# Optimization experiments

Hardware: AMD Instinct MI355X
Metric: run time of the kernel (lower is better)

Reference implementation:

```python
import jax, jax.numpy as jnp
import numpy as np

B, IN, H1, H2, OUT, P = 8192, 1024, 2048, 2048, 1024, 8


def setup_inputs() -> dict:
    key = jax.random.key(0)
    ks = jax.random.split(key, 12)
    s = 0.02
    return {
        "x": jax.random.normal(ks[0], (B, IN), dtype=jnp.float32),
        # layer 1: P expert linears (stacked) + selector
        "W1": jax.random.normal(ks[1], (P, IN, H1), dtype=jnp.float32) * s,
        "b1": jax.random.normal(ks[2], (P, H1), dtype=jnp.float32) * s,
        "S1": jax.random.normal(ks[3], (IN, P), dtype=jnp.float32) * s,
        "sb1": jax.random.normal(ks[4], (P,), dtype=jnp.float32) * s,
        # layer 2
        "W2": jax.random.normal(ks[5], (P, H1, H2), dtype=jnp.float32) * s,
        "b2": jax.random.normal(ks[6], (P, H2), dtype=jnp.float32) * s,
        "S2": jax.random.normal(ks[7], (H1, P), dtype=jnp.float32) * s,
        "sb2": jax.random.normal(ks[8], (P,), dtype=jnp.float32) * s,
        # classifier
        "Wc": jax.random.normal(ks[9], (H2, OUT), dtype=jnp.float32) * s,
        "bc": jax.random.normal(ks[10], (OUT,), dtype=jnp.float32) * s,
    }


def _drn_layer(x, W, b, S, sb):
    # selector + softmax routing probs: [B, P]
    probs = jax.nn.softmax(x @ S + sb, axis=-1)
    # all-expert dense outputs: [B, P, O]
    outs = jnp.einsum('bi,pio->bpo', x, W) + b[None, :, :]
    # soft-weighted combine over experts
    return jnp.einsum('bpo,bp->bo', outs, probs)


def reference(x, W1, b1, S1, sb1, W2, b2, S2, sb2, Wc, bc):
    h = jax.nn.relu(_drn_layer(x, W1, b1, S1, sb1))
    h = jax.nn.relu(_drn_layer(h, W2, b2, S2, sb2))
    return h @ Wc + bc
```

## Files before the change

kernel.cpp:

```cpp
#include <hip/hip_runtime.h>
#include <hip/hip_bf16.h>

#define B_SZ   8192
#define IN_SZ  1024
#define H1_SZ  2048
#define H2_SZ  2048
#define OUT_SZ 1024
#define NP     8

typedef __bf16 bf16x8 __attribute__((ext_vector_type(8)));
typedef float  f32x4  __attribute__((ext_vector_type(4)));

__device__ __forceinline__ void async_ld16(const void* g, void* l) {
    __builtin_amdgcn_global_load_lds(
        (const __attribute__((address_space(1))) unsigned int*)g,
        (__attribute__((address_space(3))) unsigned int*)l,
        16, 0, 0);
}

__device__ __forceinline__ void transpose_body(float (*tile)[33],
                                               const float* __restrict__ in,
                                               __hip_bfloat16* __restrict__ out,
                                               int K, int N, int bx, int by) {
    int n0 = bx * 32, k0 = by * 32;
    int tx = threadIdx.x, ty = threadIdx.y;
#pragma unroll
    for (int j = 0; j < 4; ++j)
        tile[ty + j * 8][tx] = in[(size_t)(k0 + ty + j * 8) * N + (n0 + tx)];
    __syncthreads();
    const int kk = (tx & 15) * 2;
#pragma unroll
    for (int j = 0; j < 2; ++j) {
        int nn = ty + j * 8 + (tx >> 4) * 16;
        __hip_bfloat16 t2[2] = {__float2bfloat16(tile[kk][nn]),
                                __float2bfloat16(tile[kk + 1][nn])};
        unsigned int u;
        __builtin_memcpy(&u, t2, 4);
        *(unsigned int*)(out + (size_t)(n0 + nn) * K + (k0 + kk)) = u;
    }
}

__global__ void prep_k(const float* __restrict__ W1, const float* __restrict__ W2,
                       const float* __restrict__ Wc, const float* __restrict__ x,
                       __hip_bfloat16* __restrict__ W1t, __hip_bfloat16* __restrict__ W2t,
                       __hip_bfloat16* __restrict__ Wct, __hip_bfloat16* __restrict__ xbf) {
    __shared__ float tile[32][33];
    int id = blockIdx.x;
    const int nA = (H1_SZ / 32) * ((NP * IN_SZ) / 32);
    const int nB = (H2_SZ / 32) * ((NP * H1_SZ) / 32);
    const int nC = (OUT_SZ / 32) * (H2_SZ / 32);
    if (id < nA) {
        transpose_body(tile, W1, W1t, NP * IN_SZ, H1_SZ, id % (H1_SZ / 32), id / (H1_SZ / 32));
        return;
    }
    id -= nA;
    if (id < nB) {
        transpose_body(tile, W2, W2t, NP * H1_SZ, H2_SZ, id % (H2_SZ / 32), id / (H2_SZ / 32));
        return;
    }
    id -= nB;
    if (id < nC) {
        transpose_body(tile, Wc, Wct, H2_SZ, OUT_SZ, id % (OUT_SZ / 32), id / (OUT_SZ / 32));
        return;
    }
    id -= nC;
    {
        int t = threadIdx.y * 32 + threadIdx.x;
        size_t i = ((size_t)id * 256 + t) * 8;
        float4 f0 = *(const float4*)(x + i);
        float4 f1 = *(const float4*)(x + i + 4);
        __hip_bfloat16 tt[8] = {
            __float2bfloat16(f0.x), __float2bfloat16(f0.y),
            __float2bfloat16(f0.z), __float2bfloat16(f0.w),
            __float2bfloat16(f1.x), __float2bfloat16(f1.y),
            __float2bfloat16(f1.z), __float2bfloat16(f1.w)};
        uint4 u4;
        __builtin_memcpy(&u4, tt, 16);
        *(uint4*)(xbf + i) = u4;
    }
}

template <typename T>
__global__ void selector_k(const T* __restrict__ in, const float* __restrict__ S,
                           const float* __restrict__ sb, float* __restrict__ probs,
                           float* __restrict__ ratT, int K) {
    int row  = blockIdx.x * blockDim.y + threadIdx.y;
    int lane = threadIdx.x;
    float acc[NP];
#pragma unroll
    for (int p = 0; p < NP; ++p) acc[p] = 0.f;
    const T* xr = in + (size_t)row * K;
    for (int k = lane; k < K; k += 64) {
        float xv;
        if constexpr (sizeof(T) == 2) xv = __bfloat162float(xr[k]);
        else                          xv = (float)xr[k];
        const float* sr = S + (size_t)k * NP;
#pragma unroll
        for (int p = 0; p < NP; ++p) acc[p] += xv * sr[p];
    }
#pragma unroll
    for (int p = 0; p < NP; ++p)
#pragma unroll
        for (int off = 32; off > 0; off >>= 1)
            acc[p] += __shfl_down(acc[p], off, 64);
    if (lane == 0) {
        float v[NP], m = -1e30f;
#pragma unroll
        for (int p = 0; p < NP; ++p) { v[p] = acc[p] + sb[p]; m = fmaxf(m, v[p]); }
        float s = 0.f;
#pragma unroll
        for (int p = 0; p < NP; ++p) { v[p] = expf(v[p] - m); s += v[p]; }
        float inv = 1.f / s;
#pragma unroll
        for (int p = 0; p < NP; ++p) probs[(size_t)row * NP + p] = v[p] * inv;
#pragma unroll
        for (int p = 0; p < NP - 1; ++p) ratT[(size_t)p * B_SZ + row] = v[p] / v[p + 1];
        ratT[(size_t)(NP - 1) * B_SZ + row] = v[NP - 1] * inv;
    }
}

template <int TPS>
__global__ __launch_bounds__(512, 2)
void drn_gemm8_k(const __hip_bfloat16* __restrict__ A, const __hip_bfloat16* __restrict__ Wt,
                 int N, int K, int Kin, const float* __restrict__ ratT,
                 const float* __restrict__ probs, const float* __restrict__ bexp,
                 __hip_bfloat16* __restrict__ C) {
    __shared__ alignas(16) char smem[131072];

    const int tid  = threadIdx.x;
    const int wid  = tid >> 6, lane = tid & 63;
    const int quad = lane >> 4, l16 = lane & 15;
    const int wr = wid >> 2, wc = wid & 3;

    const int g   = blockIdx.x;
    const int cpx = gridDim.x >> 3;
    const int wg  = (g & 7) * cpx + (g >> 3);
    const int nbn = N >> 8;
    const int mb  = wg / nbn, nb = wg % nbn;
    const int m0  = mb * 256, n0 = nb * 256;

    const int arow = tid >> 3;
    const int gsw  = ((tid & 7) ^ (arow & 7)) << 3;
    const __hip_bfloat16* Ag = A  + (size_t)(m0 + arow) * Kin + gsw;
    const __hip_bfloat16* Bg = Wt + (size_t)(n0 + arow) * K + gsw;
    const size_t r64a = (size_t)64 * Kin;
    const size_t r64b = (size_t)64 * K;
    char* aDst = smem + wid * 1024;
    char* bDst = smem + 65536 + wid * 1024;

#define STG_A(dbuf, ksrc, h) do {                                              \
    const __hip_bfloat16* s_ = Ag + (((ksrc) & (TPS - 1)) * 64) + (size_t)(2*(h)) * r64a; \
    char* d_ = aDst + (dbuf) * 32768 + (h) * 16384;                            \
    async_ld16(s_,        d_);                                                 \
    async_ld16(s_ + r64a, d_ + 8192); } while (0)
#define STG_B(dbuf, ksrc, h) do {                                              \
    const __hip_bfloat16* s_ = Bg + ((size_t)(ksrc) * 64) + (size_t)(2*(h)) * r64b; \
    char* d_ = bDst + (dbuf) * 32768 + (h) * 16384;                            \
    async_ld16(s_,        d_);                                                 \
    async_ld16(s_ + r64b, d_ + 8192); } while (0)

    const int csw  = (quad ^ (l16 & 7)) << 4;
    const int aoff = (wr * 128 + l16) * 128 + csw;
    const int boff = 65536 + (wc * 64 + l16) * 128 + csw;

#define LDA(dst, dbuf, m, k) dst = *(const bf16x8*)(smem + (dbuf) * 32768 + ((aoff ^ ((k) << 6)) + (m) * 2048))
#define LDB(dst, dbuf, n, k) dst = *(const bf16x8*)(smem + (dbuf) * 32768 + ((boff ^ ((k) << 6)) + (n) * 2048))

#define LD_AF(dst, dbuf, mq)                               \
    LDA(dst[0][0], dbuf, 2*(mq),     0); LDA(dst[0][1], dbuf, 2*(mq),     1); \
    LDA(dst[1][0], dbuf, 2*(mq) + 1, 0); LDA(dst[1][1], dbuf, 2*(mq) + 1, 1)
#define LD_BF(dst, dbuf, kk)                               \
    LDB(dst[0][kk], dbuf, 0, kk); LDB(dst[1][kk], dbuf, 1, kk); \
    LDB(dst[2][kk], dbuf, 2, kk); LDB(dst[3][kk], dbuf, 3, kk)

#define BAR()                                              \
    __builtin_amdgcn_s_barrier();                          \
    __builtin_amdgcn_sched_barrier(0)

#define VMW(n) asm volatile("s_waitcnt vmcnt(" #n ")" ::: "memory")

#define MF16(afX, bfrX, q) do {                            \
    __builtin_amdgcn_s_setprio(1);                         \
    _Pragma("unroll")                                      \
    for (int ml = 0; ml < 2; ++ml)                         \
      _Pragma("unroll")                                    \
      for (int n_ = 0; n_ < 4; ++n_)                       \
        _Pragma("unroll")                                  \
        for (int k_ = 0; k_ < 2; ++k_)                     \
          acc[2*(q)+ml][n_] = __builtin_amdgcn_mfma_f32_16x16x32_bf16( \
              afX[ml][k_], bfrX[n_][k_], acc[2*(q)+ml][n_], 0, 0, 0);  \
    __builtin_amdgcn_s_setprio(0); } while (0)

    f32x4 zero = {0.f, 0.f, 0.f, 0.f};
    f32x4 acc[8][4];
#pragma unroll
    for (int m = 0; m < 8; ++m)
#pragma unroll
        for (int n = 0; n < 4; ++n) acc[m][n] = zero;

    const int NT = K >> 6;
    const int NI = NT >> 1;

    STG_A(0, 0, 0); STG_A(0, 0, 1);
    STG_B(0, 0, 0); STG_B(0, 0, 1);
    STG_B(1, 1, 0); STG_B(1, 1, 1);
    VMW(4);
    BAR();
    bf16x8 afA[2][2], afB[2][2], bfrA[4][2], bfrB[4][2];
    LD_BF(bfrA, 0, 0); LD_BF(bfrA, 0, 1);
    LD_AF(afA, 0, 0);

    for (int i = 0; i < NI; ++i) {
        const int T  = 2 * i;
        const int k2 = (T + 2 < NT) ? T + 2 : NT - 1;
        const int k3 = (T + 3 < NT) ? T + 3 : NT - 1;

        STG_A(1, T + 1, 0);
        LD_AF(afB, 0, 1);
        BAR(); MF16(afA, bfrA, 0); BAR();
        STG_A(1, T + 1, 1);
        VMW(4);
        LD_AF(afA, 0, 2);
        BAR(); MF16(afB, bfrA, 1); BAR();
        STG_B(0, k2, 0);
        VMW(2);
        LD_AF(afB, 0, 3);
        LD_BF(bfrB, 1, 0);
        BAR(); MF16(afA, bfrA, 2); BAR();
        STG_B(0, k2, 1);
        LD_AF(afA, 1, 0);
        LD_BF(bfrB, 1, 1);
        BAR(); MF16(afB, bfrA, 3); BAR();
        STG_A(0, k2, 0);
        LD_AF(afB, 1, 1);
        BAR(); MF16(afA, bfrB, 0); BAR();
        STG_A(0, k2, 1);
        VMW(4);
        LD_AF(afA, 1, 2);
        BAR(); MF16(afB, bfrB, 1); BAR();
        STG_B(1, k3, 0);
        VMW(2);
        LD_AF(afB, 1, 3);
        LD_BF(bfrA, 0, 0);
        BAR(); MF16(afA, bfrB, 2); BAR();
        STG_B(1, k3, 1);
        LD_AF(afA, 0, 0);
        LD_BF(bfrA, 0, 1);
        BAR(); MF16(afB, bfrB, 3); BAR();

        if (((i + 1) & (TPS / 2 - 1)) == 0) {
            const int p = (i + 1) / (TPS / 2) - 1;
            const float* rp = ratT + (size_t)p * B_SZ + (m0 + wr * 128 + quad * 4);
            f32x4 rr[8];
#pragma unroll
            for (int m = 0; m < 8; ++m) rr[m] = *(const f32x4*)(rp + m * 16);
#pragma unroll
            for (int m = 0; m < 8; ++m)
#pragma unroll
                for (int n = 0; n < 4; ++n)
                    acc[m][n] *= rr[m];
        }
    }

    asm volatile("s_waitcnt vmcnt(0)" ::: "memory");

    const int colb = n0 + wc * 64 + l16;
    float bx[4][NP];
#pragma unroll
    for (int n = 0; n < 4; ++n)
#pragma unroll
        for (int p = 0; p < NP; ++p)
            bx[n][p] = bexp[(size_t)p * N + colb + n * 16];
#pragma unroll
    for (int m = 0; m < 8; ++m) {
#pragma unroll
        for (int r = 0; r < 4; ++r) {
            const int row = m0 + wr * 128 + m * 16 + quad * 4 + r;
            const float* pr = probs + (size_t)row * NP;
            f32x4 p0 = *(const f32x4*)pr;
            f32x4 p1 = *(const f32x4*)(pr + 4);
            float pv[NP] = {p0[0], p0[1], p0[2], p0[3], p1[0], p1[1], p1[2], p1[3]};
#pragma unroll
            for (int n = 0; n < 4; ++n) {
                float bsum = 0.f;
#pragma unroll
                for (int p = 0; p < NP; ++p) bsum += pv[p] * bx[n][p];
                float v = fmaxf(acc[m][n][r] + bsum, 0.f);
                C[(size_t)row * N + colb + n * 16] = __float2bfloat16(v);
            }
        }
    }
#undef STG_A
#undef STG_B
#undef LDA
#undef LDB
#undef LD_AF
#undef LD_BF
#undef BAR
#undef VMW
#undef MF16
}

__global__ __launch_bounds__(256)
void gemm_bt_k(const __hip_bfloat16* __restrict__ A, const __hip_bfloat16* __restrict__ Bt,
               int M, int N, int K, const float* __restrict__ bias, float* __restrict__ C) {
    __shared__ alignas(16) __hip_bfloat16 As[2 * 128 * 32];
    __shared__ alignas(16) __hip_bfloat16 Bs[2 * 128 * 32];
    const int tid  = threadIdx.x;
    const int wid  = tid >> 6, lane = tid & 63;
    const int quad = lane >> 4, l16 = lane & 15;
    const int waveM = (wid >> 1) << 6, waveN = (wid & 1) << 6;
    const int m0 = blockIdx.x * 128, n0 = blockIdx.y * 128;

    f32x4 zero = {0.f, 0.f, 0.f, 0.f};
    f32x4 acc[4][4];
#pragma unroll
    for (int a = 0; a < 4; ++a)
#pragma unroll
        for (int b = 0; b < 4; ++b) acc[a][b] = zero;

    const int srow = tid >> 2;
    const int skc  = (((tid & 3) ^ (srow & 3) ^ ((srow >> 2) & 3)) << 3);
    const __hip_bfloat16* Ag = A  + (size_t)(m0 + srow) * K + skc;
    const __hip_bfloat16* Bg = Bt + (size_t)(n0 + srow) * K + skc;
    const size_t rowStep = (size_t)64 * K;
    __hip_bfloat16* AsB = As + wid * 512;
    __hip_bfloat16* BsB = Bs + wid * 512;
    const int csel = (quad ^ (l16 & 3) ^ ((l16 >> 2) & 3)) << 3;

    async_ld16(Ag,           AsB);
    async_ld16(Ag + rowStep, AsB + 2048);
    async_ld16(Bg,           BsB);
    async_ld16(Bg + rowStep, BsB + 2048);

    for (int kt = 0; kt < K; kt += 32) {
        const int cur = (kt >> 5) & 1;
        __syncthreads();
        if (kt + 32 < K) {
            const int nb = (1 - cur) * 4096;
            async_ld16(Ag + kt + 32,           AsB + nb);
            async_ld16(Ag + kt + 32 + rowStep, AsB + nb + 2048);
            async_ld16(Bg + kt + 32,           BsB + nb);
            async_ld16(Bg + kt + 32 + rowStep, BsB + nb + 2048);
        }
        const __hip_bfloat16* AsC = As + cur * 4096;
        const __hip_bfloat16* BsC = Bs + cur * 4096;
        bf16x8 af[4], bfr[4];
#pragma unroll
        for (int q = 0; q < 4; ++q) {
            af[q]  = *(const bf16x8*)(AsC + (waveM + q * 16 + l16) * 32 + csel);
            bfr[q] = *(const bf16x8*)(BsC + (waveN + q * 16 + l16) * 32 + csel);
        }
#pragma unroll
        for (int tm = 0; tm < 4; ++tm)
#pragma unroll
            for (int tn = 0; tn < 4; ++tn)
                acc[tm][tn] = __builtin_amdgcn_mfma_f32_16x16x32_bf16(
                    af[tm], bfr[tn], acc[tm][tn], 0, 0, 0);
    }

    const int colb = n0 + waveN + l16;
#pragma unroll
    for (int tm = 0; tm < 4; ++tm)
#pragma unroll
        for (int r = 0; r < 4; ++r) {
            int row = m0 + waveM + tm * 16 + quad * 4 + r;
#pragma unroll
            for (int tn = 0; tn < 4; ++tn)
                C[(size_t)row * N + colb + tn * 16] =
                    acc[tm][tn][r] + bias[colb + tn * 16];
        }
}

extern "C" void kernel_launch(void* const* d_in, const int* in_sizes, int n_in,
                              void* d_out, int out_size, void* d_ws, size_t ws_size,
                              hipStream_t stream) {
    const float* x   = (const float*)d_in[0];
    const float* W1  = (const float*)d_in[1];
    const float* b1  = (const float*)d_in[2];
    const float* S1  = (const float*)d_in[3];
    const float* sb1 = (const float*)d_in[4];
    const float* W2  = (const float*)d_in[5];
    const float* b2  = (const float*)d_in[6];
    const float* S2  = (const float*)d_in[7];
    const float* sb2 = (const float*)d_in[8];
    const float* Wc  = (const float*)d_in[9];
    const float* bc  = (const float*)d_in[10];
    float* out = (float*)d_out;

    char* ws = (char*)d_ws;
    size_t off = 0;
    auto alloc = [&](size_t bytes) {
        char* p = ws + off;
        off += (bytes + 255) & ~(size_t)255;
        return p;
    };
    __hip_bfloat16* W1t = (__hip_bfloat16*)alloc((size_t)H1_SZ * (NP * IN_SZ) * 2);
    __hip_bfloat16* W2t = (__hip_bfloat16*)alloc((size_t)H2_SZ * (NP * H1_SZ) * 2);
    __hip_bfloat16* Wct = (__hip_bfloat16*)alloc((size_t)OUT_SZ * H2_SZ * 2);
    float* probs1       = (float*)alloc((size_t)B_SZ * NP * 4);
    float* probs2       = (float*)alloc((size_t)B_SZ * NP * 4);
    float* rat1         = (float*)alloc((size_t)NP * B_SZ * 4);
    float* rat2         = (float*)alloc((size_t)NP * B_SZ * 4);
    __hip_bfloat16* xbf = (__hip_bfloat16*)alloc((size_t)B_SZ * IN_SZ * 2);
    __hip_bfloat16* h1  = (__hip_bfloat16*)alloc((size_t)B_SZ * H1_SZ * 2);
    __hip_bfloat16* h2  = (__hip_bfloat16*)alloc((size_t)B_SZ * H2_SZ * 2);

    const int nPrep = (H1_SZ / 32) * ((NP * IN_SZ) / 32)
                    + (H2_SZ / 32) * ((NP * H1_SZ) / 32)
                    + (OUT_SZ / 32) * (H2_SZ / 32)
                    + (B_SZ * IN_SZ) / (256 * 8);
    prep_k<<<nPrep, dim3(32, 8), 0, stream>>>(W1, W2, Wc, x, W1t, W2t, Wct, xbf);

    selector_k<float><<<B_SZ / 4, dim3(64, 4), 0, stream>>>(x, S1, sb1, probs1, rat1, IN_SZ);
    drn_gemm8_k<16><<<(B_SZ / 256) * (H1_SZ / 256), 512, 0, stream>>>(
        xbf, W1t, H1_SZ, NP * IN_SZ, IN_SZ, rat1, probs1, b1, h1);

    selector_k<__hip_bfloat16><<<B_SZ / 4, dim3(64, 4), 0, stream>>>(h1, S2, sb2, probs2, rat2, H1_SZ);
    drn_gemm8_k<32><<<(B_SZ / 256) * (H2_SZ / 256), 512, 0, stream>>>(
        h1, W2t, H2_SZ, NP * H1_SZ, H1_SZ, rat2, probs2, b2, h2);

    gemm_bt_k<<<dim3(B_SZ / 128, OUT_SZ / 128), 256, 0, stream>>>(
        h2, Wct, B_SZ, OUT_SZ, H2_SZ, bc, out);
}
```

Before: 990.8 us.

## Restructure MFMA main loop into k-half phases with precomputed LDS fragment pointers

Replaces the ping-pong A/B fragment register double-buffering in the fused expert GEMM with a simpler schedule. Each tile now runs four phases, each loading 4 A fragments (plus B fragments for one k-half) and then issuing 16 MFMAs after an explicit lgkmcnt(0) wait. LDS base pointers are precomputed per buffer and k-half to cut address arithmetic, and the global-load wait points move. The aim is to lower register pressure and instruction overhead, at the cost of losing the overlap between LDS reads and MFMA issue within a wave.

```diff
diff --git a/kernel.cpp b/kernel.cpp
--- a/kernel.cpp
+++ b/kernel.cpp
@@ -159,36 +159,43 @@
     async_ld16(s_,        d_);                                                 \
     async_ld16(s_ + r64b, d_ + 8192); } while (0)
 
-    const int csw  = (quad ^ (l16 & 7)) << 4;
-    const int aoff = (wr * 128 + l16) * 128 + csw;
-    const int boff = 65536 + (wc * 64 + l16) * 128 + csw;
-
-#define LDA(dst, dbuf, m, k) dst = *(const bf16x8*)(smem + (dbuf) * 32768 + ((aoff ^ ((k) << 6)) + (m) * 2048))
-#define LDB(dst, dbuf, n, k) dst = *(const bf16x8*)(smem + (dbuf) * 32768 + ((boff ^ ((k) << 6)) + (n) * 2048))
-
-#define LD_AF(dst, dbuf, mq)                               \
-    LDA(dst[0][0], dbuf, 2*(mq),     0); LDA(dst[0][1], dbuf, 2*(mq),     1); \
-    LDA(dst[1][0], dbuf, 2*(mq) + 1, 0); LDA(dst[1][1], dbuf, 2*(mq) + 1, 1)
-#define LD_BF(dst, dbuf, kk)                               \
-    LDB(dst[0][kk], dbuf, 0, kk); LDB(dst[1][kk], dbuf, 1, kk); \
-    LDB(dst[2][kk], dbuf, 2, kk); LDB(dst[3][kk], dbuf, 3, kk)
+    const int csw   = (quad ^ (l16 & 7)) << 4;
+    const int abase = (wr * 128 + l16) * 128 + csw;
+    const int bbase = 65536 + (wc * 64 + l16) * 128 + csw;
+    const char* aB[2][2] = {{smem + abase,         smem + (abase ^ 64)},
+                            {smem + 32768 + abase, smem + 32768 + (abase ^ 64)}};
+    const char* bB[2][2] = {{smem + bbase,         smem + (bbase ^ 64)},
+                            {smem + 32768 + bbase, smem + 32768 + (bbase ^ 64)}};
+
+#define LD_A4(d, mh, kh)                                                        \
+    af[0] = *(const bf16x8*)(aB[d][kh] + ((mh) * 4 + 0) * 2048);                \
+    af[1] = *(const bf16x8*)(aB[d][kh] + ((mh) * 4 + 1) * 2048);                \
+    af[2] = *(const bf16x8*)(aB[d][kh] + ((mh) * 4 + 2) * 2048);                \
+    af[3] = *(const bf16x8*)(aB[d][kh] + ((mh) * 4 + 3) * 2048)
+#define LD_B4(d, kh)                                                            \
+    bfr[0][kh] = *(const bf16x8*)(bB[d][kh] + 0 * 2048);                        \
+    bfr[1][kh] = *(const bf16x8*)(bB[d][kh] + 1 * 2048);                        \
+    bfr[2][kh] = *(const bf16x8*)(bB[d][kh] + 2 * 2048);                        \
+    bfr[3][kh] = *(const bf16x8*)(bB[d][kh] + 3 * 2048)
 
 #define BAR()                                              \
     __builtin_amdgcn_s_barrier();                          \
     __builtin_amdgcn_sched_barrier(0)
 
+#define LGKM0()                                            \
+    asm volatile("s_waitcnt lgkmcnt(0)" ::: "memory");     \
+    __builtin_amdgcn_sched_barrier(0)
+
 #define VMW(n) asm volatile("s_waitcnt vmcnt(" #n ")" ::: "memory")
 
-#define MF16(afX, bfrX, q) do {                            \
+#define MF(mh, kh) do {                                    \
     __builtin_amdgcn_s_setprio(1);                         \
     _Pragma("unroll")                                      \
-    for (int ml = 0; ml < 2; ++ml)                         \
+    for (int ml = 0; ml < 4; ++ml)                         \
       _Pragma("unroll")                                    \
       for (int n_ = 0; n_ < 4; ++n_)                       \
-        _Pragma("unroll")                                  \
-        for (int k_ = 0; k_ < 2; ++k_)                     \
-          acc[2*(q)+ml][n_] = __builtin_amdgcn_mfma_f32_16x16x32_bf16( \
-              afX[ml][k_], bfrX[n_][k_], acc[2*(q)+ml][n_], 0, 0, 0);  \
+        acc[(mh) * 4 + ml][n_] = __builtin_amdgcn_mfma_f32_16x16x32_bf16( \
+            af[ml], bfr[n_][kh], acc[(mh) * 4 + ml][n_], 0, 0, 0);        \
     __builtin_amdgcn_s_setprio(0); } while (0)
 
     f32x4 zero = {0.f, 0.f, 0.f, 0.f};
@@ -206,47 +213,33 @@
     STG_B(1, 1, 0); STG_B(1, 1, 1);
     VMW(4);
     BAR();
-    bf16x8 afA[2][2], afB[2][2], bfrA[4][2], bfrB[4][2];
-    LD_BF(bfrA, 0, 0); LD_BF(bfrA, 0, 1);
-    LD_AF(afA, 0, 0);
+
+    bf16x8 af[4], bfr[4][2];
 
     for (int i = 0; i < NI; ++i) {
         const int T  = 2 * i;
         const int k2 = (T + 2 < NT) ? T + 2 : NT - 1;
         const int k3 = (T + 3 < NT) ? T + 3 : NT - 1;
 
-        STG_A(1, T + 1, 0);
-        LD_AF(afB, 0, 1);
-        BAR(); MF16(afA, bfrA, 0); BAR();
-        STG_A(1, T + 1, 1);
-        VMW(4);
-        LD_AF(afA, 0, 2);
-        BAR(); MF16(afB, bfrA, 1); BAR();
-        STG_B(0, k2, 0);
-        VMW(2);
-        LD_AF(afB, 0, 3);
-        LD_BF(bfrB, 1, 0);
-        BAR(); MF16(afA, bfrA, 2); BAR();
-        STG_B(0, k2, 1);
-        LD_AF(afA, 1, 0);
-        LD_BF(bfrB, 1, 1);
-        BAR(); MF16(afB, bfrA, 3); BAR();
-        STG_A(0, k2, 0);
-        LD_AF(afB, 1, 1);
-        BAR(); MF16(afA, bfrB, 0); BAR();
-        STG_A(0, k2, 1);
-        VMW(4);
-        LD_AF(afA, 1, 2);
-        BAR(); MF16(afB, bfrB, 1); BAR();
-        STG_B(1, k3, 0);
-        VMW(2);
-        LD_AF(afB, 1, 3);
-        LD_BF(bfrA, 0, 0);
-        BAR(); MF16(afA, bfrB, 2); BAR();
-        STG_B(1, k3, 1);
-        LD_AF(afA, 0, 0);
-        LD_BF(bfrA, 0, 1);
-        BAR(); MF16(afB, bfrB, 3); BAR();
+        STG_A(1, T + 1, 0); LD_B4(0, 0); LD_A4(0, 0, 0);
+        BAR(); LGKM0(); MF(0, 0); BAR();
+        STG_A(1, T + 1, 1); LD_B4(0, 1); LD_A4(0, 0, 1);
+        BAR(); LGKM0(); MF(0, 1); BAR();
+        STG_B(0, k2, 0);                 LD_A4(0, 1, 0);
+        BAR(); LGKM0(); MF(1, 0); BAR();
+        STG_B(0, k2, 1);                 LD_A4(0, 1, 1);
+        BAR(); LGKM0(); MF(1, 1);
+        VMW(4); BAR();
+
+        STG_A(0, k2, 0); LD_B4(1, 0); LD_A4(1, 0, 0);
+        BAR(); LGKM0(); MF(0, 0); BAR();
+        STG_A(0, k2, 1); LD_B4(1, 1); LD_A4(1, 0, 1);
+        BAR(); LGKM0(); MF(0, 1); BAR();
+        STG_B(1, k3, 0);              LD_A4(1, 1, 0);
+        BAR(); LGKM0(); MF(1, 0); BAR();
+        STG_B(1, k3, 1);              LD_A4(1, 1, 1);
+        BAR(); LGKM0(); MF(1, 1);
+        VMW(4); BAR();
 
         if (((i + 1) & (TPS / 2 - 1)) == 0) {
             const int p = (i + 1) / (TPS / 2) - 1;
@@ -292,13 +285,12 @@
     }
 #undef STG_A
 #undef STG_B
-#undef LDA
-#undef LDB
-#undef LD_AF
-#undef LD_BF
+#undef LD_A4
+#undef LD_B4
 #undef BAR
+#undef LGKM0
 #undef VMW
-#undef MF16
+#undef MF
 }
 
 __global__ __launch_bounds__(256)
```

Result: no change. 995.3 us (+0.5%).
